# Performance work log

Hardware: AMD Instinct MI355X
Metric: run time of the kernel (lower is better)

Reference implementation:

```python
import jax, jax.numpy as jnp
import numpy as np

IN_CH, OUT_CH, HID, NHEAD = 4, 1, 256, 8
VDIM = HID // NHEAD
LOCALITIES = (2.0, 10.0, 10.0, 10.0, 10.0, 200.0)
N_BLOCKS = len(LOCALITIES) - 2
INPUT_RES, LATENT_RES, OUTPUT_RES = (64, 64), (32, 32), (64, 64)
BATCH = 8


def pairwise_dist(res1x, res1y, res2x, res2y):
    gx1 = jnp.linspace(0, 1, res1x + 1)[:-1]
    gy1 = jnp.linspace(0, 1, res1y + 1)[:-1]
    g1x, g1y = jnp.meshgrid(gx1, gy1, indexing='xy')
    grid1 = jnp.stack([g1x.flatten(), g1y.flatten()], axis=-1)
    gx2 = jnp.linspace(0, 1, res2x + 1)[:-1]
    gy2 = jnp.linspace(0, 1, res2y + 1)[:-1]
    g2x, g2y = jnp.meshgrid(gx2, gy2, indexing='xy')
    grid2 = jnp.stack([g2x.flatten(), g2y.flatten()], axis=-1)
    diff = grid1[:, None, :] - grid2[None, :, :]
    return (jnp.sum(diff ** 2, axis=-1) / 2.0).astype(jnp.float32)


def pos_att(m_dist, x, r, w, locality):
    # m_dist:[Nq,Nk]  x:[B,Nk,HID]  r:[H,1,1]  w:[H,HID,VDIM]
    scale = jnp.tan(0.25 * jnp.pi * (1 - 1e-07) * (1 + jnp.sin(r)))
    sd = m_dist[None, :, :] * scale  # [H,Nq,Nk]
    if locality <= 100:
        thr = jnp.percentile(sd, locality, axis=-1, keepdims=True)
        sd = jnp.where(sd <= thr, sd, jnp.inf)
    att = jax.nn.softmax(-sd, axis=-1)  # [H,Nq,Nk]
    value = jnp.einsum('bnj,hjk->bhnk', x, w)  # [B,H,Nk,VDIM]
    out = jnp.einsum('hjn,bhnk->bhjk', att, value)  # [B,H,Nq,VDIM]
    out = jnp.transpose(out, (0, 2, 1, 3)).reshape(x.shape[0], m_dist.shape[0], -1)
    return jax.nn.gelu(out)


def lin(x, w, b):
    # eqx.nn.Linear: w:[out,in], b:[out]
    return jnp.einsum('bni,oi->bno', x, w) + b


def setup_inputs() -> dict:
    key = jax.random.key(0)
    ks = jax.random.split(key, 20)
    Ni = INPUT_RES[0] * INPUT_RES[1]
    s_h = 1.0 / jnp.sqrt(HID)
    s_in = 1.0 / jnp.sqrt(IN_CH)
    return {
        'x': jax.random.normal(ks[0], (BATCH, Ni, IN_CH), jnp.float32),
        'en_fc1_w': jax.random.uniform(ks[1], (HID, IN_CH), jnp.float32, -s_in, s_in),
        'en_fc1_b': jax.random.uniform(ks[2], (HID,), jnp.float32, -s_in, s_in),
        'down_r': jax.random.normal(ks[3], (NHEAD, 1, 1), jnp.float32),
        'down_w': jax.random.normal(ks[4], (NHEAD, HID, VDIM), jnp.float32) * s_h,
        'pa_r': jax.random.normal(ks[5], (N_BLOCKS, NHEAD, 1, 1), jnp.float32),
        'pa_w': jax.random.normal(ks[6], (N_BLOCKS, NHEAD, HID, VDIM), jnp.float32) * s_h,
        'mlp1_w': jax.random.uniform(ks[7], (N_BLOCKS, HID, HID), jnp.float32, -s_h, s_h),
        'mlp1_b': jax.random.uniform(ks[8], (N_BLOCKS, HID), jnp.float32, -s_h, s_h),
        'mlp2_w': jax.random.uniform(ks[9], (N_BLOCKS, HID, HID), jnp.float32, -s_h, s_h),
        'mlp2_b': jax.random.uniform(ks[10], (N_BLOCKS, HID), jnp.float32, -s_h, s_h),
        'res_w': jax.random.uniform(ks[11], (N_BLOCKS, HID, HID), jnp.float32, -s_h, s_h),
        'res_b': jax.random.uniform(ks[12], (N_BLOCKS, HID), jnp.float32, -s_h, s_h),
        'up_r': jax.random.normal(ks[13], (NHEAD, 1, 1), jnp.float32),
        'up_w': jax.random.normal(ks[14], (NHEAD, HID, VDIM), jnp.float32) * s_h,
        'de_fc1_w': jax.random.uniform(ks[15], (HID, HID), jnp.float32, -s_h, s_h),
        'de_fc1_b': jax.random.uniform(ks[16], (HID,), jnp.float32, -s_h, s_h),
        'de_fc2_w': jax.random.uniform(ks[17], (OUT_CH, HID), jnp.float32, -s_h, s_h),
        'de_fc2_b': jax.random.uniform(ks[18], (OUT_CH,), jnp.float32, -s_h, s_h),
    }


def reference(x, en_fc1_w, en_fc1_b, down_r, down_w, pa_r, pa_w,
              mlp1_w, mlp1_b, mlp2_w, mlp2_b, res_w, res_b,
              up_r, up_w, de_fc1_w, de_fc1_b, de_fc2_w, de_fc2_b):
    m_dist_down = pairwise_dist(LATENT_RES[0], LATENT_RES[1], INPUT_RES[0], INPUT_RES[1])
    m_dist_proc = pairwise_dist(LATENT_RES[0], LATENT_RES[1], LATENT_RES[0], LATENT_RES[1])
    m_dist_up = pairwise_dist(OUTPUT_RES[0], OUTPUT_RES[1], LATENT_RES[0], LATENT_RES[1])

    h = jax.nn.gelu(lin(x, en_fc1_w, en_fc1_b))
    h = pos_att(m_dist_down, h, down_r, down_w, LOCALITIES[0])
    for i in range(N_BLOCKS):
        pa_out = pos_att(m_dist_proc, h, pa_r[i], pa_w[i], LOCALITIES[1 + i])
        mlp_out = lin(jax.nn.gelu(lin(pa_out, mlp1_w[i], mlp1_b[i])), mlp2_w[i], mlp2_b[i])
        residual = lin(h, res_w[i], res_b[i])
        h = jax.nn.gelu(mlp_out + residual)
    h = pos_att(m_dist_up, h, up_r, up_w, LOCALITIES[-1])
    h = jax.nn.gelu(lin(h, de_fc1_w, de_fc1_b))
    return lin(h, de_fc2_w, de_fc2_b)
```

## Files before the change

kernel.cpp:

```cpp
#include <hip/hip_runtime.h>
#include <math.h>


#define PI_F 3.14159265358979323846f

typedef __attribute__((ext_vector_type(8))) short short8;
typedef __attribute__((ext_vector_type(4))) float float4v;
typedef __attribute__((ext_vector_type(4))) unsigned short ushort4v;

__device__ __forceinline__ float gelu_f(float x) {
  float u = 0.7978845608028654f * (x + 0.044715f * x * x * x);
  float e = __expf(2.0f * u);
  float t = 1.0f - 2.0f / (e + 1.0f);
  return 0.5f * x * (1.0f + t);
}

__device__ __forceinline__ float head_scale(float r) {
  return tanf(0.25f * PI_F * (1.0f - 1e-7f) * (1.0f + sinf(r)));
}

__device__ __forceinline__ unsigned short f2bf(float f) {
  union { float f; unsigned u; } c; c.f = f;
  unsigned u = c.u + 0x7FFFu + ((c.u >> 16) & 1u);
  return (unsigned short)(u >> 16);
}
__device__ __forceinline__ float bf2f(unsigned short h) {
  union { unsigned u; float f; } c; c.u = ((unsigned)h) << 16;
  return c.f;
}
__device__ __forceinline__ void split_bf(float f, unsigned short& hi,
                                         unsigned short& lo) {
  hi = f2bf(f);
  lo = f2bf(f - bf2f(hi));
}

__device__ __forceinline__ void gl16(const void* g, void* l) {
  __builtin_amdgcn_global_load_lds(
      (const __attribute__((address_space(1))) unsigned int*)g,
      (__attribute__((address_space(3))) unsigned int*)l, 16, 0, 0);
}

__global__ __launch_bounds__(256) void k_enc(
    const float* __restrict__ x, const float* __restrict__ w,
    const float* __restrict__ b, unsigned short* __restrict__ ahi,
    unsigned short* __restrict__ alo) {
  int row = blockIdx.x * 4 + (threadIdx.x >> 6);
  int o = (threadIdx.x & 63) * 4;
  float4 xv = *(const float4*)(x + (size_t)row * 4);
  ushort4v hv, lv;
#pragma unroll
  for (int i = 0; i < 4; ++i) {
    float4 wv = *(const float4*)(w + (size_t)(o + i) * 4);
    float s = xv.x * wv.x + xv.y * wv.y + xv.z * wv.z + xv.w * wv.w + b[o + i];
    s = gelu_f(s);
    unsigned short hi, lo;
    split_bf(s, hi, lo);
    hv[i] = hi; lv[i] = lo;
  }
  size_t idx = (size_t)row * 256 + o;
  *(ushort4v*)(ahi + idx) = hv;
  *(ushort4v*)(alo + idx) = lv;
}

__global__ __launch_bounds__(256) void k_split_all(
    const float* __restrict__ down_w, const float* __restrict__ de1_w,
    const float* __restrict__ up_w, const float* __restrict__ pa_w,
    const float* __restrict__ mlp1_w, const float* __restrict__ mlp2_w,
    const float* __restrict__ res_w, unsigned short* __restrict__ whi,
    unsigned short* __restrict__ wlo) {
  int i = blockIdx.x * 256 + threadIdx.x;
  float f;
  if (i < 65536) {
    int n = i >> 8, k = i & 255;
    f = down_w[(n >> 5) * 8192 + k * 32 + (n & 31)];
  } else if (i < 131072) {
    f = de1_w[i - 65536];
  } else if (i < 196608) {
    int j = i - 131072;
    int n = j >> 8, k = j & 255;
    f = up_w[(n >> 5) * 8192 + k * 32 + (n & 31)];
  } else if (i < 458752) {
    int j = i - 196608;
    int blk = j >> 16, r = j & 65535;
    int n = r >> 8, k = r & 255;
    f = pa_w[(size_t)blk * 65536 + (n >> 5) * 8192 + k * 32 + (n & 31)];
  } else if (i < 720896) {
    f = mlp1_w[i - 458752];
  } else if (i < 983040) {
    f = mlp2_w[i - 720896];
  } else {
    f = res_w[i - 983040];
  }
  unsigned short hi, lo;
  split_bf(f, hi, lo);
  whi[i] = hi;
  wlo[i] = lo;
}

template <int KRES, int CXM, int NPT, int TARGET, int TMAX>
__global__ __launch_bounds__(256) void k_thresh(int* __restrict__ thr) {
  __shared__ int wsum[4];
  int q = blockIdx.x, tid = threadIdx.x;
  int qx = q & 31, qy = q >> 5;
  int cx = qx * CXM, cy = qy * CXM;
  int d[NPT];
#pragma unroll
  for (int j = 0; j < NPT; ++j) {
    int k = tid * NPT + j;
    int kx = k & (KRES - 1), ky = k / KRES;
    int dx = cx - kx, dy = cy - ky;
    d[j] = dx * dx + dy * dy;
  }
  int lo = 0, hi = TMAX;
  while (lo < hi) {
    int mid = (lo + hi) >> 1;
    int c = 0;
#pragma unroll
    for (int j = 0; j < NPT; ++j) c += (d[j] <= mid) ? 1 : 0;
#pragma unroll
    for (int off = 32; off > 0; off >>= 1) c += __shfl_down(c, off, 64);
    if ((tid & 63) == 0) wsum[tid >> 6] = c;
    __syncthreads();
    int total = wsum[0] + wsum[1] + wsum[2] + wsum[3];
    __syncthreads();
    if (total >= TARGET) hi = mid; else lo = mid + 1;
  }
  if (tid == 0) thr[q] = lo;
}

template <int KRES, int CXM, int DSHIFT, int J2>
__global__ __launch_bounds__(256) void k_klist2(
    const float* __restrict__ rvec, const int* __restrict__ thr,
    int* __restrict__ klist2, int* __restrict__ kcnt2,
    float* __restrict__ wlist2) {
  __shared__ int cntS;
  __shared__ int sidx[J2];
  __shared__ int sdv[J2][4];
  __shared__ float denS[8][4];
  int tile = blockIdx.x, tid = threadIdx.x;
  int tx = tile & 15, ty = tile >> 4;
  int cxA[4], cyA[4], T[4];
#pragma unroll
  for (int i = 0; i < 4; ++i) {
    int qx = 2 * tx + (i & 1), qy = 2 * ty + (i >> 1);
    cxA[i] = qx * CXM; cyA[i] = qy * CXM;
    T[i] = thr[qy * 32 + qx];
  }
  if (tid == 0) cntS = 0;
  __syncthreads();
  int x0 = KRES - 1, x1 = 0, y0 = KRES - 1, y1 = 0;
#pragma unroll
  for (int i = 0; i < 4; ++i) {
    int rad = (int)sqrtf((float)T[i]);
    while ((rad + 1) * (rad + 1) <= T[i]) ++rad;
    while (rad > 0 && rad * rad > T[i]) --rad;
    x0 = min(x0, max(0, cxA[i] - rad));
    x1 = max(x1, min(KRES - 1, cxA[i] + rad));
    y0 = min(y0, max(0, cyA[i] - rad));
    y1 = max(y1, min(KRES - 1, cyA[i] + rad));
  }
  int W = x1 - x0 + 1, H = y1 - y0 + 1, tot = W * H;
  for (int p = tid; p < tot; p += 256) {
    int kx = x0 + p % W, ky = y0 + p / W;
    int d[4]; bool keep = false;
#pragma unroll
    for (int i = 0; i < 4; ++i) {
      int dx = cxA[i] - kx, dy = cyA[i] - ky;
      d[i] = dx * dx + dy * dy;
      keep = keep || (d[i] <= T[i]);
    }
    if (keep) {
      int s = atomicAdd(&cntS, 1);
      if (s < J2) {
        sidx[s] = ky * KRES + kx;
#pragma unroll
        for (int i = 0; i < 4; ++i) sdv[s][i] = d[i];
      }
    }
  }
  __syncthreads();
  int cnt = min(cntS, J2);
  int h = tid >> 5, lane = tid & 31;
  float sc = head_scale(rvec[h]) * (1.0f / (float)(1 << DSHIFT));
  float den[4] = {0.f, 0.f, 0.f, 0.f};
  for (int j = lane; j < cnt; j += 32) {
#pragma unroll
    for (int i = 0; i < 4; ++i)
      if (sdv[j][i] <= T[i]) den[i] += __expf(-sc * (float)sdv[j][i]);
  }
#pragma unroll
  for (int i = 0; i < 4; ++i) {
    float d0 = den[i];
#pragma unroll
    for (int off = 16; off > 0; off >>= 1) d0 += __shfl_down(d0, off, 32);
    if (lane == 0) denS[h][i] = d0;
  }
  __syncthreads();
  float inv[4];
#pragma unroll
  for (int i = 0; i < 4; ++i) inv[i] = 1.0f / denS[h][i];
  for (int j = lane; j < cnt; j += 32) {
    float w[4];
#pragma unroll
    for (int i = 0; i < 4; ++i)
      w[i] = (sdv[j][i] <= T[i]) ? __expf(-sc * (float)sdv[j][i]) * inv[i] : 0.f;
    float4v wv = {w[0], w[1], w[2], w[3]};
    *(float4v*)&wlist2[(((size_t)h * 256 + tile) * J2 + j) * 4] = wv;
  }
  if (tid == 0) kcnt2[tile] = cnt;
  if (h == 0)
    for (int j = lane; j < cnt; j += 32) klist2[(size_t)tile * J2 + j] = sidx[j];
}

template <int NK, int J2>
__global__ __launch_bounds__(256) void k_att3(
    const float* __restrict__ value,
    const int* __restrict__ klist2, const int* __restrict__ kcnt2,
    const float* __restrict__ wlist2, unsigned short* __restrict__ ohi,
    unsigned short* __restrict__ olo) {
  __shared__ int kls[J2];
  __shared__ float4v wls[J2];
  __shared__ float4v part[4][4][64];
  int blk = blockIdx.x;
  int tile = blk >> 3, h = blk & 7;
  int tid = threadIdx.x, g = tid & 63, s = tid >> 6;
  int cnt = kcnt2[tile];
  for (int j = tid; j < cnt; j += 256) {
    kls[j] = klist2[(size_t)tile * J2 + j];
    wls[j] = *(const float4v*)&wlist2[(((size_t)h * 256 + tile) * J2 + j) * 4];
  }
  __syncthreads();
  const float* vb = value + (size_t)h * NK * 256 + g * 4;
  float4v acc[4];
#pragma unroll
  for (int i = 0; i < 4; ++i) acc[i] = (float4v)0.0f;
  for (int j = s; j < cnt; j += 4) {
    int row = kls[j];
    float4v v = *(const float4v*)(vb + (size_t)row * 256);
    float4v w = wls[j];
    acc[0] += w.x * v;
    acc[1] += w.y * v;
    acc[2] += w.z * v;
    acc[3] += w.w * v;
  }
#pragma unroll
  for (int i = 0; i < 4; ++i) part[s][i][g] = acc[i];
  __syncthreads();
  if (tid < 64) {
    int g2 = tid;
    int ttx = tile & 15, tty = tile >> 4;
    int batch = g2 >> 3, v0 = (g2 & 7) * 4;
#pragma unroll
    for (int i = 0; i < 4; ++i) {
      float4v o4 = part[0][i][g2] + part[1][i][g2] + part[2][i][g2] +
                   part[3][i][g2];
      int q = (2 * tty + (i >> 1)) * 32 + 2 * ttx + (i & 1);
      size_t idx = ((size_t)batch * 1024 + q) * 256 + h * 32 + v0;
      ushort4v hv, lv;
#pragma unroll
      for (int c = 0; c < 4; ++c) {
        float oo = gelu_f(o4[c]);
        unsigned short hi, lo;
        split_bf(oo, hi, lo);
        hv[c] = hi; lv[c] = lo;
      }
      *(ushort4v*)(ohi + idx) = hv;
      *(ushort4v*)(olo + idx) = lv;
    }
  }
}

template <int BM, int BN, bool DUAL, int OL, bool GEL, bool OHILO>
__global__ __launch_bounds__(256) void k_gw(
    const unsigned short* __restrict__ A1hi, const unsigned short* __restrict__ A1lo,
    const unsigned short* __restrict__ W1hi, const unsigned short* __restrict__ W1lo,
    const unsigned short* __restrict__ A2hi, const unsigned short* __restrict__ A2lo,
    const unsigned short* __restrict__ W2hi, const unsigned short* __restrict__ W2lo,
    const float* __restrict__ bias, const float* __restrict__ bias2,
    float* __restrict__ outf, unsigned short* __restrict__ ohi,
    unsigned short* __restrict__ olo, int NS) {
  constexpr int MS = BM / 32;
  constexpr int NF = BN / 32;
  constexpr int NWR = BN / 8;
  __shared__ alignas(16) unsigned short Wh_s[BN * 256];
  __shared__ alignas(16) unsigned short Wl_s[BN * 256];
  int tid = threadIdx.x;
  int b = blockIdx.x;
  int x = b & 7, t = b >> 3;
  int nq = t & 3, mt = (t >> 2) * 8 + x;
  int m0 = mt * BM, n_off = nq * BN;
  int w = tid >> 6, lane = tid & 63;
  int quad = lane >> 4, l16 = lane & 15;
  int wm = (w >> 1) * (BM / 2), wn = (w & 1) * (BN / 2);

  int wgo[NWR], wls_[NWR];
#pragma unroll
  for (int i = 0; i < NWR; ++i) {
    int rem = tid + i * 256;
    int r = rem >> 5, s = rem & 31, c = s ^ (r & 7);
    wgo[i] = (n_off + r) * 256 + c * 8;
    wls_[i] = rem * 8;
  }

  float4v acc[MS][NF];
#pragma unroll
  for (int i = 0; i < MS; ++i)
#pragma unroll
    for (int n = 0; n < NF; ++n) acc[i][n] = (float4v)0.0f;

  const int NPASS = DUAL ? 2 : 1;
  for (int p = 0; p < NPASS; ++p) {
    const unsigned short* pWh = p ? W2hi : W1hi;
    const unsigned short* pWl = p ? W2lo : W1lo;
    const unsigned short* pAh = p ? A2hi : A1hi;
    const unsigned short* pAl = p ? A2lo : A1lo;
    if (p) __syncthreads();
#pragma unroll
    for (int i = 0; i < NWR; ++i) {
      gl16(pWh + wgo[i], &Wh_s[wls_[i]]);
      gl16(pWl + wgo[i], &Wl_s[wls_[i]]);
    }
    __syncthreads();
#pragma unroll
    for (int ks2 = 0; ks2 < 8; ++ks2) {
      short8 ah[MS], al[MS];
#pragma unroll
      for (int ms = 0; ms < MS; ++ms) {
        size_t off = (size_t)(m0 + wm + ms * 16 + l16) * 256 + ks2 * 32 +
                     quad * 8;
        ah[ms] = *(const short8*)(pAh + off);
        al[ms] = *(const short8*)(pAl + off);
      }
#pragma unroll
      for (int ns = 0; ns < NF; ++ns) {
        int lr = wn + ns * 16 + l16;
        int L = ks2 * 4 + quad;
        int so = lr * 256 + (L ^ (lr & 7)) * 8;
        short8 bh = *(const short8*)&Wh_s[so];
        short8 bl = *(const short8*)&Wl_s[so];
#pragma unroll
        for (int ms = 0; ms < MS; ++ms) {
          acc[ms][ns] = __builtin_amdgcn_mfma_f32_16x16x32_bf16(
              ah[ms], bh, acc[ms][ns], 0, 0, 0);
          acc[ms][ns] = __builtin_amdgcn_mfma_f32_16x16x32_bf16(
              ah[ms], bl, acc[ms][ns], 0, 0, 0);
          acc[ms][ns] = __builtin_amdgcn_mfma_f32_16x16x32_bf16(
              al[ms], bh, acc[ms][ns], 0, 0, 0);
        }
      }
    }
  }
#pragma unroll
  for (int ms = 0; ms < MS; ++ms) {
#pragma unroll
    for (int ns = 0; ns < NF; ++ns) {
      int n = n_off + wn + ns * 16 + l16;
      float bv = bias ? bias[n] : 0.0f;
      if (DUAL && bias2) bv += bias2[n];
#pragma unroll
      for (int r = 0; r < 4; ++r) {
        int m = m0 + wm + ms * 16 + quad * 4 + r;
        float c = acc[ms][ns][r] + bv;
        if (GEL) c = gelu_f(c);
        if (OHILO) {
          unsigned short chi, clo;
          split_bf(c, chi, clo);
          ohi[(size_t)m * 256 + n] = chi;
          olo[(size_t)m * 256 + n] = clo;
        } else if (OL == 0) {
          outf[(size_t)m * 256 + n] = c;
        } else {
          int N = 1 << NS;
          int bb = m >> NS, rr = m & (N - 1);
          outf[(((size_t)(n >> 5) * N + rr) * 8 + bb) * 32 + (n & 31)] = c;
        }
      }
    }
  }
}

__global__ __launch_bounds__(256) void k_up_s1(
    const float* __restrict__ value,
    const float* __restrict__ rvec, float* __restrict__ T) {
  __shared__ float AxL[64][33];
  int ky = blockIdx.x, h = blockIdx.y, tid = threadIdx.x;
  float sc = head_scale(rvec[h]) * (1.0f / 8192.0f);
  float v[32];
  const float* vb = value + ((size_t)h * 1024 + ky * 32) * 256 + tid;
#pragma unroll
  for (int kx = 0; kx < 32; ++kx) v[kx] = vb[kx * 256];
  if (tid < 64) {
    int qx = tid, dxmin = qx & 1;
    for (int kx = 0; kx < 32; ++kx) {
      int dx = qx - 2 * kx;
      AxL[qx][kx] = __expf(-sc * (float)(dx * dx - dxmin));
    }
  }
  __syncthreads();
  float* tb = T + (((size_t)h * 64) * 32 + ky) * 256 + tid;
  for (int qx = 0; qx < 64; ++qx) {
    float acc = 0.f;
#pragma unroll
    for (int kx = 0; kx < 32; ++kx) acc += AxL[qx][kx] * v[kx];
    tb[(size_t)qx * 32 * 256] = acc;
  }
}

__global__ __launch_bounds__(256) void k_up_s2(
    const float* __restrict__ T, const float* __restrict__ rvec,
    unsigned short* __restrict__ ohi, unsigned short* __restrict__ olo) {
  __shared__ float AyL[64][33];
  __shared__ float Sy[64];
  __shared__ float SxS;
  int qx = blockIdx.x, h = blockIdx.y, tid = threadIdx.x;
  float sc = head_scale(rvec[h]) * (1.0f / 8192.0f);
  float t[32];
  const float* tb = T + ((size_t)h * 64 + qx) * 32 * 256 + tid;
#pragma unroll
  for (int ky = 0; ky < 32; ++ky) t[ky] = tb[ky * 256];
  if (tid < 64) {
    int qy = tid, dymin = qy & 1;
    float s = 0.f;
    for (int ky = 0; ky < 32; ++ky) {
      int dy = qy - 2 * ky;
      float e = __expf(-sc * (float)(dy * dy - dymin));
      AyL[qy][ky] = e;
      s += e;
    }
    Sy[qy] = s;
  } else if (tid >= 64 && tid < 96) {
    int kx = tid - 64, dxmin = qx & 1;
    int dx = qx - 2 * kx;
    float e = __expf(-sc * (float)(dx * dx - dxmin));
#pragma unroll
    for (int off = 16; off > 0; off >>= 1) e += __shfl_down(e, off, 32);
    if (kx == 0) SxS = e;
  }
  __syncthreads();
  float invSx = 1.0f / SxS;
  int b = tid >> 5, v = tid & 31;
  size_t base = ((size_t)b * 4096 + qx) * 256 + h * 32 + v;
  for (int qy = 0; qy < 64; ++qy) {
    float acc = 0.f;
#pragma unroll
    for (int ky = 0; ky < 32; ++ky) acc += AyL[qy][ky] * t[ky];
    float o = gelu_f(acc * invSx / Sy[qy]);
    unsigned short hi, lo;
    split_bf(o, hi, lo);
    size_t idx = base + (size_t)qy * 64 * 256;
    ohi[idx] = hi;
    olo[idx] = lo;
  }
}

__global__ __launch_bounds__(256) void k_fc2(const float* __restrict__ h,
                                             const float* __restrict__ w,
                                             const float* __restrict__ b,
                                             float* __restrict__ out) {
  int row = blockIdx.x * 4 + (threadIdx.x >> 6);
  int lane = threadIdx.x & 63;
  float4 hv = *(const float4*)(h + (size_t)row * 256 + lane * 4);
  float4 wv = *(const float4*)(w + lane * 4);
  float s = hv.x * wv.x + hv.y * wv.y + hv.z * wv.z + hv.w * wv.w;
#pragma unroll
  for (int off = 32; off > 0; off >>= 1) s += __shfl_down(s, off, 64);
  if (lane == 0) out[row] = s + b[0];
}

extern "C" void kernel_launch(void* const* d_in, const int* in_sizes, int n_in,
                              void* d_out, int out_size, void* d_ws,
                              size_t ws_size, hipStream_t stream) {
  const float* x      = (const float*)d_in[0];
  const float* en_w   = (const float*)d_in[1];
  const float* en_b   = (const float*)d_in[2];
  const float* down_r = (const float*)d_in[3];
  const float* down_w = (const float*)d_in[4];
  const float* pa_r   = (const float*)d_in[5];
  const float* pa_w   = (const float*)d_in[6];
  const float* mlp1_w = (const float*)d_in[7];
  const float* mlp1_b = (const float*)d_in[8];
  const float* mlp2_w = (const float*)d_in[9];
  const float* mlp2_b = (const float*)d_in[10];
  const float* res_w  = (const float*)d_in[11];
  const float* res_b  = (const float*)d_in[12];
  const float* up_r   = (const float*)d_in[13];
  const float* up_w   = (const float*)d_in[14];
  const float* de1_w  = (const float*)d_in[15];
  const float* de1_b  = (const float*)d_in[16];
  const float* de2_w  = (const float*)d_in[17];
  const float* de2_b  = (const float*)d_in[18];
  float* out = (float*)d_out;

  constexpr int J2 = 256;
  float* ws = (float*)d_ws;
  unsigned short* Ahi = (unsigned short*)ws;
  unsigned short* Alo = Ahi + 8388608;
  float* B = ws + 8388608;
  float* Tbuf = B + 2097152;
  unsigned short* hAhi = (unsigned short*)(ws + 16777216);
  unsigned short* hAlo = hAhi + 2097152;
  unsigned short* hBhi = hAlo + 2097152;
  unsigned short* hBlo = hBhi + 2097152;
  unsigned short* pahi = hBlo + 2097152;
  unsigned short* palo = pahi + 2097152;
  unsigned short* m1hi = palo + 2097152;
  unsigned short* m1lo = m1hi + 2097152;
  int* thrD = (int*)(ws + 25165824);
  int* thrP = thrD + 1024;
  int* cntD2 = thrP + 1024;
  int* cntP2 = cntD2 + 256;
  int* klD2 = cntP2 + 256;
  int* klP2 = klD2 + 256 * J2;
  float* wlD2 = (float*)(klP2 + 256 * J2);
  float* wlP2 = wlD2 + 2097152;
  unsigned short* Whi = (unsigned short*)(wlP2 + 2097152);
  unsigned short* Wlo = Whi + 1245184;
  const int WO_DOWN = 0, WO_DE1 = 65536, WO_UP = 131072, WO_PA = 196608,
            WO_MLP1 = 458752, WO_MLP2 = 720896, WO_RES = 983040;

  k_enc<<<8192, 256, 0, stream>>>(x, en_w, en_b, Ahi, Alo);
  k_split_all<<<4864, 256, 0, stream>>>(down_w, de1_w, up_w, pa_w, mlp1_w,
                                        mlp2_w, res_w, Whi, Wlo);
  k_thresh<64, 2, 16, 82, 7938><<<1024, 256, 0, stream>>>(thrD);
  k_thresh<32, 1, 4, 103, 1922><<<1024, 256, 0, stream>>>(thrP);
  k_klist2<64, 2, 13, J2><<<256, 256, 0, stream>>>(down_r, thrD, klD2, cntD2,
                                                   wlD2);
  k_klist2<32, 1, 11, J2><<<256, 256, 0, stream>>>(pa_r, thrP, klP2, cntP2,
                                                   wlP2);
  k_gw<128, 64, false, 1, false, false><<<1024, 256, 0, stream>>>(
      Ahi, Alo, Whi + WO_DOWN, Wlo + WO_DOWN, nullptr, nullptr, nullptr,
      nullptr, nullptr, nullptr, B, nullptr, nullptr, 12);
  k_att3<4096, J2><<<2048, 256, 0, stream>>>(B, klD2, cntD2, wlD2, hAhi, hAlo);
  for (int i = 0; i < 4; ++i) {
    const unsigned short* hih = (i & 1) ? hBhi : hAhi;
    const unsigned short* hil = (i & 1) ? hBlo : hAlo;
    unsigned short* hoh = (i & 1) ? hAhi : hBhi;
    unsigned short* hol = (i & 1) ? hAlo : hBlo;
    k_gw<64, 64, false, 1, false, false><<<512, 256, 0, stream>>>(
        hih, hil, Whi + WO_PA + i * 65536, Wlo + WO_PA + i * 65536, nullptr,
        nullptr, nullptr, nullptr, nullptr, nullptr, B, nullptr, nullptr, 10);
    k_att3<1024, J2><<<2048, 256, 0, stream>>>(B, klP2, cntP2, wlP2, pahi,
                                               palo);
    k_gw<64, 64, false, 0, true, true><<<512, 256, 0, stream>>>(
        pahi, palo, Whi + WO_MLP1 + i * 65536, Wlo + WO_MLP1 + i * 65536,
        nullptr, nullptr, nullptr, nullptr, mlp1_b + i * 256, nullptr, nullptr,
        m1hi, m1lo, 0);
    k_gw<64, 64, true, 0, true, true><<<512, 256, 0, stream>>>(
        m1hi, m1lo, Whi + WO_MLP2 + i * 65536, Wlo + WO_MLP2 + i * 65536, hih,
        hil, Whi + WO_RES + i * 65536, Wlo + WO_RES + i * 65536,
        mlp2_b + i * 256, res_b + i * 256, nullptr, hoh, hol, 0);
  }
  k_gw<64, 64, false, 1, false, false><<<512, 256, 0, stream>>>(
      hAhi, hAlo, Whi + WO_UP, Wlo + WO_UP, nullptr, nullptr, nullptr, nullptr,
      nullptr, nullptr, B, nullptr, nullptr, 10);
  k_up_s1<<<dim3(32, 8), 256, 0, stream>>>(B, up_r, Tbuf);
  k_up_s2<<<dim3(64, 8), 256, 0, stream>>>(Tbuf, up_r, Ahi, Alo);
  k_gw<128, 64, false, 0, true, false><<<1024, 256, 0, stream>>>(
      Ahi, Alo, Whi + WO_DE1, Wlo + WO_DE1, nullptr, nullptr, nullptr, nullptr,
      de1_b, nullptr, B, nullptr, nullptr, 0);
  k_fc2<<<8192, 256, 0, stream>>>(B, de2_w, de2_b, out);
}
```

Before: 559.4 us.

## Store activations and weights in MFMA-fragment tiled layout, drop LDS staging in GEMM

```diff
diff --git a/kernel.cpp b/kernel.cpp
--- a/kernel.cpp
+++ b/kernel.cpp
@@ -34,10 +34,9 @@
   lo = f2bf(f - bf2f(hi));
 }
 
-__device__ __forceinline__ void gl16(const void* g, void* l) {
-  __builtin_amdgcn_global_load_lds(
-      (const __attribute__((address_space(1))) unsigned int*)g,
-      (__attribute__((address_space(3))) unsigned int*)l, 16, 0, 0);
+__device__ __forceinline__ size_t taddr(int row, int k) {
+  return (size_t)(row >> 4) * 4096 + ((k >> 3) << 7) + ((row & 15) << 3) +
+         (k & 7);
 }
 
 __global__ __launch_bounds__(256) void k_enc(
@@ -57,9 +56,9 @@
     split_bf(s, hi, lo);
     hv[i] = hi; lv[i] = lo;
   }
-  size_t idx = (size_t)row * 256 + o;
-  *(ushort4v*)(ahi + idx) = hv;
-  *(ushort4v*)(alo + idx) = lv;
+  size_t ti = taddr(row, o);
+  *(ushort4v*)(ahi + ti) = hv;
+  *(ushort4v*)(alo + ti) = lv;
 }
 
 __global__ __launch_bounds__(256) void k_split_all(
@@ -70,31 +69,42 @@
     unsigned short* __restrict__ wlo) {
   int i = blockIdx.x * 256 + threadIdx.x;
   float f;
+  int base, n, k;
   if (i < 65536) {
-    int n = i >> 8, k = i & 255;
+    n = i >> 8; k = i & 255; base = 0;
     f = down_w[(n >> 5) * 8192 + k * 32 + (n & 31)];
   } else if (i < 131072) {
-    f = de1_w[i - 65536];
+    int j = i - 65536; n = j >> 8; k = j & 255; base = 65536;
+    f = de1_w[j];
   } else if (i < 196608) {
-    int j = i - 131072;
-    int n = j >> 8, k = j & 255;
+    int j = i - 131072; n = j >> 8; k = j & 255; base = 131072;
     f = up_w[(n >> 5) * 8192 + k * 32 + (n & 31)];
   } else if (i < 458752) {
     int j = i - 196608;
     int blk = j >> 16, r = j & 65535;
-    int n = r >> 8, k = r & 255;
+    n = r >> 8; k = r & 255; base = 196608 + blk * 65536;
     f = pa_w[(size_t)blk * 65536 + (n >> 5) * 8192 + k * 32 + (n & 31)];
   } else if (i < 720896) {
-    f = mlp1_w[i - 458752];
+    int j = i - 458752;
+    int blk = j >> 16, r = j & 65535;
+    n = r >> 8; k = r & 255; base = 458752 + blk * 65536;
+    f = mlp1_w[j];
   } else if (i < 983040) {
-    f = mlp2_w[i - 720896];
+    int j = i - 720896;
+    int blk = j >> 16, r = j & 65535;
+    n = r >> 8; k = r & 255; base = 720896 + blk * 65536;
+    f = mlp2_w[j];
   } else {
-    f = res_w[i - 983040];
+    int j = i - 983040;
+    int blk = j >> 16, r = j & 65535;
+    n = r >> 8; k = r & 255; base = 983040 + blk * 65536;
+    f = res_w[j];
   }
   unsigned short hi, lo;
   split_bf(f, hi, lo);
-  whi[i] = hi;
-  wlo[i] = lo;
+  size_t ti = (size_t)base + taddr(n, k);
+  whi[ti] = hi;
+  wlo[ti] = lo;
 }
 
 template <int KRES, int CXM, int NPT, int TARGET, int TMAX>
@@ -255,7 +265,8 @@
       float4v o4 = part[0][i][g2] + part[1][i][g2] + part[2][i][g2] +
                    part[3][i][g2];
       int q = (2 * tty + (i >> 1)) * 32 + 2 * ttx + (i & 1);
-      size_t idx = ((size_t)batch * 1024 + q) * 256 + h * 32 + v0;
+      int row = batch * 1024 + q;
+      int kk = h * 32 + v0;
       ushort4v hv, lv;
 #pragma unroll
       for (int c = 0; c < 4; ++c) {
@@ -264,14 +275,15 @@
         split_bf(oo, hi, lo);
         hv[c] = hi; lv[c] = lo;
       }
-      *(ushort4v*)(ohi + idx) = hv;
-      *(ushort4v*)(olo + idx) = lv;
-    }
-  }
-}
-
-template <int BM, int BN, bool DUAL, int OL, bool GEL, bool OHILO>
-__global__ __launch_bounds__(256) void k_gw(
+      size_t ti = taddr(row, kk);
+      *(ushort4v*)(ohi + ti) = hv;
+      *(ushort4v*)(olo + ti) = lv;
+    }
+  }
+}
+
+template <int MSW, bool DUAL, int OL, bool GEL, bool OHILO>
+__global__ __launch_bounds__(256) void k_gt(
     const unsigned short* __restrict__ A1hi, const unsigned short* __restrict__ A1lo,
     const unsigned short* __restrict__ W1hi, const unsigned short* __restrict__ W1lo,
     const unsigned short* __restrict__ A2hi, const unsigned short* __restrict__ A2lo,
@@ -279,81 +291,64 @@
     const float* __restrict__ bias, const float* __restrict__ bias2,
     float* __restrict__ outf, unsigned short* __restrict__ ohi,
     unsigned short* __restrict__ olo, int NS) {
-  constexpr int MS = BM / 32;
-  constexpr int NF = BN / 32;
-  constexpr int NWR = BN / 8;
-  __shared__ alignas(16) unsigned short Wh_s[BN * 256];
-  __shared__ alignas(16) unsigned short Wl_s[BN * 256];
-  int tid = threadIdx.x;
+  constexpr int BM = MSW * 32;
   int b = blockIdx.x;
   int x = b & 7, t = b >> 3;
   int nq = t & 3, mt = (t >> 2) * 8 + x;
-  int m0 = mt * BM, n_off = nq * BN;
+  int m0 = mt * BM, n_off = nq * 64;
+  int tid = threadIdx.x;
   int w = tid >> 6, lane = tid & 63;
   int quad = lane >> 4, l16 = lane & 15;
-  int wm = (w >> 1) * (BM / 2), wn = (w & 1) * (BN / 2);
-
-  int wgo[NWR], wls_[NWR];
-#pragma unroll
-  for (int i = 0; i < NWR; ++i) {
-    int rem = tid + i * 256;
-    int r = rem >> 5, s = rem & 31, c = s ^ (r & 7);
-    wgo[i] = (n_off + r) * 256 + c * 8;
-    wls_[i] = rem * 8;
-  }
-
-  float4v acc[MS][NF];
-#pragma unroll
-  for (int i = 0; i < MS; ++i)
-#pragma unroll
-    for (int n = 0; n < NF; ++n) acc[i][n] = (float4v)0.0f;
-
-  const int NPASS = DUAL ? 2 : 1;
-  for (int p = 0; p < NPASS; ++p) {
-    const unsigned short* pWh = p ? W2hi : W1hi;
-    const unsigned short* pWl = p ? W2lo : W1lo;
-    const unsigned short* pAh = p ? A2hi : A1hi;
-    const unsigned short* pAl = p ? A2lo : A1lo;
-    if (p) __syncthreads();
-#pragma unroll
-    for (int i = 0; i < NWR; ++i) {
-      gl16(pWh + wgo[i], &Wh_s[wls_[i]]);
-      gl16(pWl + wgo[i], &Wl_s[wls_[i]]);
-    }
-    __syncthreads();
-#pragma unroll
-    for (int ks2 = 0; ks2 < 8; ++ks2) {
-      short8 ah[MS], al[MS];
-#pragma unroll
-      for (int ms = 0; ms < MS; ++ms) {
-        size_t off = (size_t)(m0 + wm + ms * 16 + l16) * 256 + ks2 * 32 +
-                     quad * 8;
-        ah[ms] = *(const short8*)(pAh + off);
-        al[ms] = *(const short8*)(pAl + off);
+  int wm = (w >> 1) * (BM / 2), wn = (w & 1) * 32;
+
+  int atile0 = (m0 + wm) >> 4;
+  int wtile0 = (n_off + wn) >> 4;
+  size_t lanoff = (size_t)lane * 8;
+
+  float4v acc[MSW][2];
+#pragma unroll
+  for (int i = 0; i < MSW; ++i)
+#pragma unroll
+    for (int n = 0; n < 2; ++n) acc[i][n] = (float4v)0.0f;
+
+  const int NSTEP = DUAL ? 16 : 8;
+#pragma unroll
+  for (int st = 0; st < NSTEP; ++st) {
+    const unsigned short *pAh, *pAl, *pWh, *pWl;
+    if (DUAL && st >= 8) { pAh = A2hi; pAl = A2lo; pWh = W2hi; pWl = W2lo; }
+    else { pAh = A1hi; pAl = A1lo; pWh = W1hi; pWl = W1lo; }
+    int ks2 = st & 7;
+    size_t ko = (size_t)ks2 * 512 + lanoff;
+    short8 bh[2], bl[2];
+#pragma unroll
+    for (int ns = 0; ns < 2; ++ns) {
+      size_t wb = (size_t)(wtile0 + ns) * 4096 + ko;
+      bh[ns] = *(const short8*)(pWh + wb);
+      bl[ns] = *(const short8*)(pWl + wb);
+    }
+    short8 ah[MSW], al[MSW];
+#pragma unroll
+    for (int ms = 0; ms < MSW; ++ms) {
+      size_t ab = (size_t)(atile0 + ms) * 4096 + ko;
+      ah[ms] = *(const short8*)(pAh + ab);
+      al[ms] = *(const short8*)(pAl + ab);
+    }
+#pragma unroll
+    for (int ms = 0; ms < MSW; ++ms)
+#pragma unroll
+      for (int ns = 0; ns < 2; ++ns) {
+        acc[ms][ns] = __builtin_amdgcn_mfma_f32_16x16x32_bf16(
+            ah[ms], bh[ns], acc[ms][ns], 0, 0, 0);
+        acc[ms][ns] = __builtin_amdgcn_mfma_f32_16x16x32_bf16(
+            ah[ms], bl[ns], acc[ms][ns], 0, 0, 0);
+        acc[ms][ns] = __builtin_amdgcn_mfma_f32_16x16x32_bf16(
+            al[ms], bh[ns], acc[ms][ns], 0, 0, 0);
       }
-#pragma unroll
-      for (int ns = 0; ns < NF; ++ns) {
-        int lr = wn + ns * 16 + l16;
-        int L = ks2 * 4 + quad;
-        int so = lr * 256 + (L ^ (lr & 7)) * 8;
-        short8 bh = *(const short8*)&Wh_s[so];
-        short8 bl = *(const short8*)&Wl_s[so];
-#pragma unroll
-        for (int ms = 0; ms < MS; ++ms) {
-          acc[ms][ns] = __builtin_amdgcn_mfma_f32_16x16x32_bf16(
-              ah[ms], bh, acc[ms][ns], 0, 0, 0);
-          acc[ms][ns] = __builtin_amdgcn_mfma_f32_16x16x32_bf16(
-              ah[ms], bl, acc[ms][ns], 0, 0, 0);
-          acc[ms][ns] = __builtin_amdgcn_mfma_f32_16x16x32_bf16(
-              al[ms], bh, acc[ms][ns], 0, 0, 0);
-        }
-      }
-    }
-  }
-#pragma unroll
-  for (int ms = 0; ms < MS; ++ms) {
-#pragma unroll
-    for (int ns = 0; ns < NF; ++ns) {
+  }
+#pragma unroll
+  for (int ms = 0; ms < MSW; ++ms) {
+#pragma unroll
+    for (int ns = 0; ns < 2; ++ns) {
       int n = n_off + wn + ns * 16 + l16;
       float bv = bias ? bias[n] : 0.0f;
       if (DUAL && bias2) bv += bias2[n];
@@ -365,8 +360,9 @@
         if (OHILO) {
           unsigned short chi, clo;
           split_bf(c, chi, clo);
-          ohi[(size_t)m * 256 + n] = chi;
-          olo[(size_t)m * 256 + n] = clo;
+          size_t ti = taddr(m, n);
+          ohi[ti] = chi;
+          olo[ti] = clo;
         } else if (OL == 0) {
           outf[(size_t)m * 256 + n] = c;
         } else {
@@ -439,7 +435,7 @@
   __syncthreads();
   float invSx = 1.0f / SxS;
   int b = tid >> 5, v = tid & 31;
-  size_t base = ((size_t)b * 4096 + qx) * 256 + h * 32 + v;
+  int kk = h * 32 + v;
   for (int qy = 0; qy < 64; ++qy) {
     float acc = 0.f;
 #pragma unroll
@@ -447,9 +443,10 @@
     float o = gelu_f(acc * invSx / Sy[qy]);
     unsigned short hi, lo;
     split_bf(o, hi, lo);
-    size_t idx = base + (size_t)qy * 64 * 256;
-    ohi[idx] = hi;
-    olo[idx] = lo;
+    int row = b * 4096 + qy * 64 + qx;
+    size_t ti = taddr(row, kk);
+    ohi[ti] = hi;
+    olo[ti] = lo;
   }
 }
 
@@ -527,7 +524,7 @@
                                                    wlD2);
   k_klist2<32, 1, 11, J2><<<256, 256, 0, stream>>>(pa_r, thrP, klP2, cntP2,
                                                    wlP2);
-  k_gw<128, 64, false, 1, false, false><<<1024, 256, 0, stream>>>(
+  k_gt<4, false, 1, false, false><<<1024, 256, 0, stream>>>(
       Ahi, Alo, Whi + WO_DOWN, Wlo + WO_DOWN, nullptr, nullptr, nullptr,
       nullptr, nullptr, nullptr, B, nullptr, nullptr, 12);
   k_att3<4096, J2><<<2048, 256, 0, stream>>>(B, klD2, cntD2, wlD2, hAhi, hAlo);
@@ -536,26 +533,26 @@
     const unsigned short* hil = (i & 1) ? hBlo : hAlo;
     unsigned short* hoh = (i & 1) ? hAhi : hBhi;
     unsigned short* hol = (i & 1) ? hAlo : hBlo;
-    k_gw<64, 64, false, 1, false, false><<<512, 256, 0, stream>>>(
+    k_gt<2, false, 1, false, false><<<512, 256, 0, stream>>>(
         hih, hil, Whi + WO_PA + i * 65536, Wlo + WO_PA + i * 65536, nullptr,
         nullptr, nullptr, nullptr, nullptr, nullptr, B, nullptr, nullptr, 10);
     k_att3<1024, J2><<<2048, 256, 0, stream>>>(B, klP2, cntP2, wlP2, pahi,
                                                palo);
-    k_gw<64, 64, false, 0, true, true><<<512, 256, 0, stream>>>(
+    k_gt<2, false, 0, true, true><<<512, 256, 0, stream>>>(
         pahi, palo, Whi + WO_MLP1 + i * 65536, Wlo + WO_MLP1 + i * 65536,
         nullptr, nullptr, nullptr, nullptr, mlp1_b + i * 256, nullptr, nullptr,
         m1hi, m1lo, 0);
-    k_gw<64, 64, true, 0, true, true><<<512, 256, 0, stream>>>(
+    k_gt<2, true, 0, true, true><<<512, 256, 0, stream>>>(
         m1hi, m1lo, Whi + WO_MLP2 + i * 65536, Wlo + WO_MLP2 + i * 65536, hih,
         hil, Whi + WO_RES + i * 65536, Wlo + WO_RES + i * 65536,
         mlp2_b + i * 256, res_b + i * 256, nullptr, hoh, hol, 0);
   }
-  k_gw<64, 64, false, 1, false, false><<<512, 256, 0, stream>>>(
+  k_gt<2, false, 1, false, false><<<512, 256, 0, stream>>>(
       hAhi, hAlo, Whi + WO_UP, Wlo + WO_UP, nullptr, nullptr, nullptr, nullptr,
       nullptr, nullptr, B, nullptr, nullptr, 10);
   k_up_s1<<<dim3(32, 8), 256, 0, stream>>>(B, up_r, Tbuf);
   k_up_s2<<<dim3(64, 8), 256, 0, stream>>>(Tbuf, up_r, Ahi, Alo);
-  k_gw<128, 64, false, 0, true, false><<<1024, 256, 0, stream>>>(
+  k_gt<4, false, 0, true, false><<<1024, 256, 0, stream>>>(
       Ahi, Alo, Whi + WO_DE1, Wlo + WO_DE1, nullptr, nullptr, nullptr, nullptr,
       de1_b, nullptr, B, nullptr, nullptr, 0);
   k_fc2<<<8192, 256, 0, stream>>>(B, de2_w, de2_b, out);
```

New measurement: 535.1 us. 4.3% less time.
